# Kernel tuning notes

Hardware: AMD Instinct MI355X
Metric: run time of the kernel (lower is better)

Reference implementation:

```python
import jax, jax.numpy as jnp
import numpy as np

D_MODEL, D_STATE, EXPAND = 1024, 16, 2
D_INNER = EXPAND * D_MODEL
BATCH, SEQ = 4, 4096


def setup_inputs() -> dict:
    key = jax.random.key(0)
    ks = jax.random.split(key, 9)
    s = 0.02
    return {
        "x": jax.random.normal(ks[0], (BATCH, SEQ, D_MODEL), jnp.float32),
        # torch Linear weight [out,in] stored transposed here as [in,out]
        "W_in": jax.random.normal(ks[1], (D_MODEL, 2 * D_INNER), jnp.float32) * s,
        "conv_w": jax.random.normal(ks[2], (D_INNER, 1, 3), jnp.float32) * s,  # depthwise, groups=D_INNER
        "conv_b": jax.random.normal(ks[3], (D_INNER,), jnp.float32) * s,
        "W_B": jax.random.normal(ks[4], (D_INNER, D_STATE), jnp.float32) * s,
        "W_C": jax.random.normal(ks[5], (D_INNER, D_STATE), jnp.float32) * s,
        "A": jax.random.normal(ks[6], (D_STATE,), jnp.float32),
        "D": jnp.ones((D_INNER,), jnp.float32),
        "W_out": jax.random.normal(ks[7], (D_INNER, D_MODEL), jnp.float32) * s,
    }


def reference(x, W_in, conv_w, conv_b, W_B, W_C, A, D, W_out):
    d_inner = conv_w.shape[0]
    # input projection and split into main / residual gate paths
    xr = jnp.einsum("bld,de->ble", x, W_in)  # [B, L, 2*d_inner]
    x_main, res = xr[..., :d_inner], xr[..., d_inner:]
    # depthwise conv1d along seq (kernel 3, pad 1)
    xc = jax.lax.conv_general_dilated(
        x_main.transpose(0, 2, 1), conv_w, (1,), [(1, 1)],
        dimension_numbers=("NCH", "OIH", "NCH"), feature_group_count=d_inner)
    xc = (xc + conv_b[None, :, None]).transpose(0, 2, 1)  # [B, L, d_inner]
    xc = jax.nn.silu(xc)
    # selective-scan inputs
    Bt = jnp.einsum("bli,is->bls", xc, W_B)  # [B, L, d_state]
    Ct = jnp.einsum("bli,is->bls", xc, W_C)
    decay = jnp.exp(-jax.nn.softplus(A))  # exp(A_diag), [d_state]

    def step(state, bc):
        b_t, c_t = bc
        state = state * decay + b_t  # i=0: zeros*decay + B[0] == B[0]
        return state, jnp.sum(state * c_t, axis=-1)  # scalar per batch

    _, ys = jax.lax.scan(step, jnp.zeros_like(Bt[:, 0]),
                         (Bt.transpose(1, 0, 2), Ct.transpose(1, 0, 2)))
    ys = ys.T  # [B, L]
    y = ys[..., None] + xc * D  # broadcast scan output across d_inner
    y = y * jax.nn.silu(res)
    return jnp.einsum("bli,id->bld", y, W_out)
```

## Files before the change

### kernel.cpp

```cpp
#include <hip/hip_runtime.h>


typedef _Float16 half8 __attribute__((ext_vector_type(8)));
typedef float floatx4 __attribute__((ext_vector_type(4)));

#define D_MODEL 1024
#define D_INNER 2048
#define SEQ     4096
#define NBATCH  4
#define NROWS   (NBATCH * SEQ)
#define CHUNK   16
#define NCHUNK  (SEQ / CHUNK)
#define NTASK   (NBATCH * NCHUNK)

__device__ __forceinline__ void async16(_Float16* lds, const _Float16* g) {
    __builtin_amdgcn_global_load_lds((const __attribute__((address_space(1))) void*)g,
                                     (__attribute__((address_space(3))) void*)lds, 16, 0, 0);
}

__device__ __forceinline__ float siluf(float x) {
    return x / (1.f + __expf(-x));
}

__device__ __forceinline__ float decay_of(const float* A, int s) {
    return __expf(-log1pf(__expf(A[s])));
}


__global__ __launch_bounds__(256) void convert_f32_f16(const float* __restrict__ src,
                                                       _Float16* __restrict__ dst) {
    size_t idx = ((size_t)blockIdx.x * 256 + threadIdx.x) * 8;
    float4 a = *(const float4*)(src + idx);
    float4 b = *(const float4*)(src + idx + 4);
    half8 o = {(_Float16)a.x, (_Float16)a.y, (_Float16)a.z, (_Float16)a.w,
               (_Float16)b.x, (_Float16)b.y, (_Float16)b.z, (_Float16)b.w};
    *(half8*)(dst + idx) = o;
}

__global__ __launch_bounds__(256) void transpose_to_f16(const float* __restrict__ src,
                                                        _Float16* __restrict__ dst,
                                                        int K, int N) {
    __shared__ float tile[32][33];
    int n0 = blockIdx.x * 32, k0 = blockIdx.y * 32;
    int x = threadIdx.x, y = threadIdx.y;
#pragma unroll
    for (int r = 0; r < 32; r += 8)
        tile[y + r][x] = src[(size_t)(k0 + y + r) * N + (n0 + x)];
    __syncthreads();
#pragma unroll
    for (int r = 0; r < 32; r += 8)
        dst[(size_t)(n0 + y + r) * K + (k0 + x)] = (_Float16)tile[x][y + r];
}

__global__ __launch_bounds__(256) void convert_wbct(const float* __restrict__ WB,
                                                    const float* __restrict__ WC,
                                                    _Float16* __restrict__ WBCT) {
    int idx = blockIdx.x * 256 + threadIdx.x;
    int n = idx >> 11, k = idx & 2047;
    float v = (n < 16) ? WB[k * 16 + n] : WC[k * 16 + (n - 16)];
    WBCT[idx] = (_Float16)v;
}


__device__ __forceinline__ void stage_half(const _Float16* __restrict__ src, int K,
                                           int rowBase, int k0, _Float16* ldsHalf) {
    const int tid = threadIdx.x;
    const int sr = tid >> 3, wid = tid >> 6;
    const int lc = ((tid & 7) ^ (sr & 7)) << 3;
#pragma unroll
    for (int r = 0; r < 2; r++) {
        const _Float16* g = src + (size_t)(rowBase + r * 64 + sr) * K + (k0 + lc);
        async16(ldsHalf + r * 4096 + wid * 512, g);
    }
}

__device__ __forceinline__ void loadA8(half8 af[4][2], const _Float16* p,
                                       int sw0, int sw1) {
#pragma unroll
    for (int m = 0; m < 4; m++) {
        af[m][0] = *(const half8*)(p + m * 1024 + sw0);
        af[m][1] = *(const half8*)(p + m * 1024 + sw1);
    }
}

__device__ __forceinline__ void loadB4(half8 bf[2][2], const _Float16* p,
                                       int sw0, int sw1) {
#pragma unroll
    for (int n = 0; n < 2; n++) {
        bf[n][0] = *(const half8*)(p + n * 1024 + sw0);
        bf[n][1] = *(const half8*)(p + n * 1024 + sw1);
    }
}

#define GP_MMA(CB, BF)                                                                  \
    __builtin_amdgcn_s_barrier();                                                       \
    __builtin_amdgcn_s_setprio(1);                                                      \
    _Pragma("unroll") for (int s = 0; s < 2; s++)                                       \
        _Pragma("unroll") for (int m = 0; m < 4; m++)                                   \
            _Pragma("unroll") for (int n = 0; n < 2; n++)                               \
                acc[m][(CB) * 2 + n] = __builtin_amdgcn_mfma_f32_16x16x32_f16(          \
                    af[m][s], (BF)[n][s], acc[m][(CB) * 2 + n], 0, 0, 0);               \
    __builtin_amdgcn_s_setprio(0);                                                      \
    __builtin_amdgcn_s_barrier();

template <typename OutT, int NC, int RT>
__global__ __launch_bounds__(512, 2) void gemm256(const _Float16* __restrict__ A,
                                                  const _Float16* __restrict__ BT,
                                                  OutT* __restrict__ C,
                                                  int M, int N, int K) {
    __shared__ __align__(16) _Float16 smem[4 * 16384];
    _Float16* const AsBase = smem;
    _Float16* const BsBase = smem + 32768;

    const int tid = threadIdx.x;
    const int wid = tid >> 6, lane = tid & 63;
    const int wm = wid >> 1, wn = wid & 1;
    const int fr = lane & 15, q = lane >> 4, frq = fr & 7;
    const int sw0 = (q ^ frq) << 3;
    const int sw1 = ((4 + q) ^ frq) << 3;
    const int aB0 = (wm * 64 + fr) * 64;
    const int bB0 = (wn * 128 + fr) * 64;

    const int b = blockIdx.x;
    const int col0 = (b % NC) * 256;
    const int rowBase = (b / NC) * (RT * 256);
    const int NT = K >> 6;

    half8 af[4][2], bfA[2][2], bfB[2][2];

    stage_half(A,  K, rowBase,       0, AsBase);
    stage_half(A,  K, rowBase + 128, 0, AsBase + 8192);
    stage_half(BT, K, col0,          0, BsBase);
    stage_half(BT, K, col0 + 128,    0, BsBase + 8192);
    stage_half(A,  K, rowBase,      64, AsBase + 16384);
    asm volatile("s_waitcnt vmcnt(2)" ::: "memory");
    __builtin_amdgcn_s_barrier();
    asm volatile("" ::: "memory");
    loadB4(bfA, BsBase + bB0, sw0, sw1);
    loadA8(af, AsBase + aB0, sw0, sw1);

    for (int rt = 0; rt < RT; ++rt) {
        const int row0 = rowBase + rt * 256;
        floatx4 acc[4][8] = {};

        for (int t = 0; t < NT; ++t) {
            _Float16* Ab  = AsBase + ((t & 1) << 14);
            _Float16* Bb  = BsBase + ((t & 1) << 14);
            _Float16* Abn = AsBase + (((t + 1) & 1) << 14);
            _Float16* Bbn = BsBase + (((t + 1) & 1) << 14);
            const int k1 = (t + 1) << 6, k2 = (t + 2) << 6;
            const bool s1 = (t + 1) < NT, s2 = (t + 2) < NT;

            loadB4(bfB, Bb + bB0 + 2048, sw0, sw1);
            if (s1) {
                stage_half(A,  K, row0 + 128, k1, Abn + 8192);
                stage_half(BT, K, col0,       k1, Bbn);
            }
            GP_MMA(0, bfA);

            loadB4(bfA, Bb + bB0 + 4096, sw0, sw1);
            if (s1) stage_half(BT, K, col0 + 128, k1, Bbn + 8192);
            GP_MMA(1, bfB);

            loadB4(bfB, Bb + bB0 + 6144, sw0, sw1);
            if (s2) stage_half(A, K, row0, k2, Ab);
            GP_MMA(2, bfA);

            if (s2) {
                asm volatile("s_waitcnt vmcnt(2)" ::: "memory");
            } else if (s1) {
                asm volatile("s_waitcnt vmcnt(0)" ::: "memory");
            }
            __builtin_amdgcn_s_barrier();
            asm volatile("" ::: "memory");
            if (s1) loadB4(bfA, Bbn + bB0, sw0, sw1);
            __builtin_amdgcn_s_setprio(1);
#pragma unroll
            for (int s = 0; s < 2; s++)
#pragma unroll
                for (int m = 0; m < 4; m++)
#pragma unroll
                    for (int n = 0; n < 2; n++)
                        acc[m][6 + n] = __builtin_amdgcn_mfma_f32_16x16x32_f16(
                            af[m][s], bfB[n][s], acc[m][6 + n], 0, 0, 0);
            __builtin_amdgcn_s_setprio(0);
            if (s1) loadA8(af, Abn + aB0, sw0, sw1);
            __builtin_amdgcn_s_barrier();
        }

        if (rt + 1 < RT) {
            const int row0n = row0 + 256;
            stage_half(A,  K, row0n,       0, AsBase);
            stage_half(A,  K, row0n + 128, 0, AsBase + 8192);
            stage_half(BT, K, col0,        0, BsBase);
            stage_half(BT, K, col0 + 128,  0, BsBase + 8192);
            stage_half(A,  K, row0n,      64, AsBase + 16384);
            asm volatile("s_waitcnt vmcnt(2)" ::: "memory");
            __builtin_amdgcn_s_barrier();
            asm volatile("" ::: "memory");
            loadB4(bfA, BsBase + bB0, sw0, sw1);
            loadA8(af, AsBase + aB0, sw0, sw1);
        }

        const int er = (lane >> 4) * 4, ec = lane & 15;
#pragma unroll
        for (int mi = 0; mi < 4; mi++)
#pragma unroll
            for (int cj = 0; cj < 8; cj++)
#pragma unroll
                for (int r = 0; r < 4; r++) {
                    int row = row0 + wm * 64 + mi * 16 + er + r;
                    int col = col0 + wn * 128 + cj * 16 + ec;
                    C[(size_t)row * N + col] = (OutT)acc[mi][cj][r];
                }
    }
}

__global__ __launch_bounds__(256) void conv_bc_fin(const _Float16* __restrict__ xr,
                                                   const float* __restrict__ cw,
                                                   const float* __restrict__ cb,
                                                   const _Float16* __restrict__ WBCT,
                                                   const float* __restrict__ A,
                                                   _Float16* __restrict__ xc,
                                                   float* __restrict__ BtCt,
                                                   float* __restrict__ fin) {
    __shared__ __align__(16) _Float16 As[4 * 32 * 128];
    const int tid = threadIdx.x, wid = tid >> 6, lane = tid & 63;
    const int row0 = blockIdx.x * 32;
    const int l0 = row0 & (SEQ - 1);
    const int cg = lane & 15;
    const int rg = lane >> 4;
    const int fr = lane & 15, q = lane >> 4;
    _Float16* As_w = As + wid * 4096;
    const int r0 = rg * 8;

    floatx4 acc[2][2] = {};

    for (int t = 0; t < 4; t++) {
        const int kbase = wid * 512 + t * 128;
        const int gcol = kbase + cg * 8;
        float w0[8], w1[8], w2[8], bb[8];
#pragma unroll
        for (int j = 0; j < 8; j++) {
            w0[j] = cw[(gcol + j) * 3];
            w1[j] = cw[(gcol + j) * 3 + 1];
            w2[j] = cw[(gcol + j) * 3 + 2];
            bb[j] = cb[gcol + j];
        }
        half8 prev = {}, cur, nxt;
        if (!(l0 == 0 && rg == 0))
            prev = *(const half8*)(xr + (size_t)(row0 + r0 - 1) * 4096 + gcol);
        cur = *(const half8*)(xr + (size_t)(row0 + r0) * 4096 + gcol);
#pragma unroll
        for (int r = 0; r < 8; r++) {
            if (r == 7 && rg == 3 && l0 + 32 == SEQ) {
                half8 z = {};
                nxt = z;
            } else {
                nxt = *(const half8*)(xr + (size_t)(row0 + r0 + r + 1) * 4096 + gcol);
            }
            half8 o;
#pragma unroll
            for (int j = 0; j < 8; j++) {
                float a = (float)prev[j] * w0[j] + (float)cur[j] * w1[j] +
                          (float)nxt[j] * w2[j] + bb[j];
                o[j] = (_Float16)siluf(a);
            }
            const int lrow = r0 + r;
            *(half8*)(xc + (size_t)(row0 + lrow) * D_INNER + gcol) = o;
            *(half8*)(As_w + lrow * 128 + ((cg ^ (lrow & 7)) * 8)) = o;
            prev = cur;
            cur = nxt;
        }
#pragma unroll
        for (int ks = 0; ks < 4; ks++) {
            half8 af[2], bf[2];
#pragma unroll
            for (int rt = 0; rt < 2; rt++)
                af[rt] = *(const half8*)(As_w + (rt * 16 + fr) * 128 +
                                         (((ks * 4 + q) ^ (fr & 7)) * 8));
#pragma unroll
            for (int ot = 0; ot < 2; ot++)
                bf[ot] = *(const half8*)(WBCT + (size_t)(ot * 16 + fr) * D_INNER +
                                         kbase + ks * 32 + q * 8);
#pragma unroll
            for (int rt = 0; rt < 2; rt++)
#pragma unroll
                for (int ot = 0; ot < 2; ot++)
                    acc[rt][ot] = __builtin_amdgcn_mfma_f32_16x16x32_f16(af[rt], bf[ot], acc[rt][ot], 0, 0, 0);
        }
    }

    __syncthreads();
    float* red = (float*)As;
    float* btl = (float*)As + 4096;
    const int er = (lane >> 4) * 4, ec = lane & 15;
#pragma unroll
    for (int rt = 0; rt < 2; rt++)
#pragma unroll
        for (int ot = 0; ot < 2; ot++)
#pragma unroll
            for (int rr = 0; rr < 4; rr++)
                red[wid * 1024 + (rt * 16 + er + rr) * 32 + ot * 16 + ec] = acc[rt][ot][rr];
    __syncthreads();
#pragma unroll
    for (int i = 0; i < 4; i++) {
        int idx = i * 256 + tid;
        float v = red[idx] + red[1024 + idx] + red[2048 + idx] + red[3072 + idx];
        btl[idx] = v;
        BtCt[(size_t)row0 * 32 + idx] = v;
    }
    __syncthreads();
    if (tid < 32) {
        const int ch = tid >> 4, s = tid & 15;
        const float decay = decay_of(A, s);
        float st = 0.f;
#pragma unroll
        for (int r = 0; r < CHUNK; r++)
            st = st * decay + btl[(ch * 16 + r) * 32 + s];
        fin[((row0 >> 4) + ch) * 16 + s] = st;
    }
}

__global__ __launch_bounds__(64) void scan_p2(const float* __restrict__ fin,
                                              const float* __restrict__ A,
                                              float* __restrict__ carry) {
    int t = threadIdx.x;
    int b = t >> 4, s = t & 15;
    float decay = decay_of(A, s);
    float d16 = decay;
#pragma unroll
    for (int k = 0; k < 4; k++) d16 *= d16;
    float cy = 0.f;
#pragma unroll 8
    for (int c = 0; c < NCHUNK; c++) {
        int idx = ((b * NCHUNK) + c) * 16 + s;
        carry[idx] = cy;
        cy = cy * d16 + fin[idx];
    }
}

__global__ __launch_bounds__(256) void scan_p3_fuse(const float* __restrict__ BtCt,
                                                    const float* __restrict__ A,
                                                    const float* __restrict__ carry,
                                                    const float* __restrict__ D,
                                                    const _Float16* __restrict__ xr,
                                                    _Float16* __restrict__ xc) {
    __shared__ float ysl[CHUNK];
    const int task = blockIdx.x;
    const int b = task >> 8, c = task & (NCHUNK - 1);
    const int row0 = b * SEQ + c * CHUNK;
    const int tid = threadIdx.x;

    if (tid < 16) {
        const int s = tid;
        const float decay = decay_of(A, s);
        size_t r = (size_t)row0 * 32;
        float bt[CHUNK], ct[CHUNK];
#pragma unroll
        for (int j = 0; j < CHUNK; j++) {
            bt[j] = BtCt[r + (size_t)j * 32 + s];
            ct[j] = BtCt[r + (size_t)j * 32 + 16 + s];
        }
        float st = carry[task * 16 + s];
        float yv[CHUNK];
#pragma unroll
        for (int j = 0; j < CHUNK; j++) {
            st = st * decay + bt[j];
            yv[j] = st * ct[j];
        }
#pragma unroll
        for (int j = 0; j < CHUNK; j++) {
            float y = yv[j];
            y += __shfl_xor(y, 1, 16);
            y += __shfl_xor(y, 2, 16);
            y += __shfl_xor(y, 4, 16);
            y += __shfl_xor(y, 8, 16);
            if (s == 0) ysl[j] = y;
        }
    }
    __syncthreads();

#pragma unroll
    for (int it = 0; it < 16; it++) {
        int chunk = it * 256 + tid;
        int rl = chunk >> 8;
        int colb = (chunk & 255) * 8;
        size_t row = (size_t)(row0 + rl);
        float yv = ysl[rl];
        half8 x8 = *(const half8*)(xc + row * D_INNER + colb);
        half8 r8 = *(const half8*)(xr + row * 4096 + 2048 + colb);
        float4 d0 = *(const float4*)(D + colb);
        float4 d1 = *(const float4*)(D + colb + 4);
        half8 o;
        float dd[8] = {d0.x, d0.y, d0.z, d0.w, d1.x, d1.y, d1.z, d1.w};
#pragma unroll
        for (int j = 0; j < 8; j++) {
            float y = yv + (float)x8[j] * dd[j];
            o[j] = (_Float16)(y * siluf((float)r8[j]));
        }
        *(half8*)(xc + row * D_INNER + colb) = o;
    }
}

extern "C" void kernel_launch(void* const* d_in, const int* in_sizes, int n_in,
                              void* d_out, int out_size, void* d_ws, size_t ws_size,
                              hipStream_t stream) {
    const float* x      = (const float*)d_in[0];
    const float* W_in   = (const float*)d_in[1];
    const float* conv_w = (const float*)d_in[2];
    const float* conv_b = (const float*)d_in[3];
    const float* W_B    = (const float*)d_in[4];
    const float* W_C    = (const float*)d_in[5];
    const float* A      = (const float*)d_in[6];
    const float* D      = (const float*)d_in[7];
    const float* W_out  = (const float*)d_in[8];
    float* out = (float*)d_out;

    char* ws = (char*)d_ws;
    size_t off = 0;
    auto alloc = [&](size_t bytes) { size_t o = off; off += (bytes + 255) & ~(size_t)255; return o; };
    _Float16* xh    = (_Float16*)(ws + alloc((size_t)NROWS * D_MODEL * 2));
    _Float16* WinT  = (_Float16*)(ws + alloc((size_t)4096 * 1024 * 2));
    _Float16* WoutT = (_Float16*)(ws + alloc((size_t)1024 * 2048 * 2));
    _Float16* WBCT  = (_Float16*)(ws + alloc((size_t)32 * 2048 * 2));
    _Float16* xr    = (_Float16*)(ws + alloc((size_t)NROWS * 4096 * 2));
    _Float16* xc    = (_Float16*)(ws + alloc((size_t)NROWS * D_INNER * 2));
    float*    BtCt  = (float*)(ws + alloc((size_t)NROWS * 32 * 4));
    float*    fin   = (float*)(ws + alloc((size_t)NTASK * 16 * 4));
    float*    carry = (float*)(ws + alloc((size_t)NTASK * 16 * 4));

    convert_f32_f16<<<(NROWS * D_MODEL) / (256 * 8), 256, 0, stream>>>(x, xh);
    transpose_to_f16<<<dim3(4096 / 32, 1024 / 32), dim3(32, 8), 0, stream>>>(W_in, WinT, 1024, 4096);
    transpose_to_f16<<<dim3(1024 / 32, 2048 / 32), dim3(32, 8), 0, stream>>>(W_out, WoutT, 2048, 1024);
    convert_wbct<<<(32 * 2048) / 256, 256, 0, stream>>>(W_B, W_C, WBCT);
    gemm256<_Float16, 16, 4><<<256, 512, 0, stream>>>(xh, WinT, xr, NROWS, 4096, 1024);
    conv_bc_fin<<<NROWS / 32, 256, 0, stream>>>(xr, conv_w, conv_b, WBCT, A, xc, BtCt, fin);
    scan_p2<<<1, 64, 0, stream>>>(fin, A, carry);
    scan_p3_fuse<<<NTASK, 256, 0, stream>>>(BtCt, A, carry, D, xr, xc);
    gemm256<float, 4, 1><<<256, 512, 0, stream>>>(xc, WoutT, out, NROWS, 1024, 2048);
}
```

Measured before the change: 428.1 us.

## Restructure GEMM main loop into two half-tile MMA phases with unified fragments

The GEMM inner loop moves from four MMA phases with ping-pong B fragment registers and cross-iteration prefetch of A/B fragments to two phases. Each phase loads a 4-wide B fragment set, and A fragments are loaded at the start of each k-tile instead of prefetched from the previous one. Barriers become inline-asm s_barrier, and the epilogue store now runs before restaging for the next row tile. This lowers register pressure and barrier count, but LDS fragment loads are no longer overlapped with the prior tile's MFMAs.

```diff
diff --git a/kernel.cpp b/kernel.cpp
--- a/kernel.cpp
+++ b/kernel.cpp
@@ -26,6 +26,8 @@
     return __expf(-log1pf(__expf(A[s])));
 }
 
+#define BAR() asm volatile("s_barrier" ::: "memory")
+
 
 __global__ __launch_bounds__(256) void convert_f32_f16(const float* __restrict__ src,
                                                        _Float16* __restrict__ dst) {
@@ -83,25 +85,25 @@
     }
 }
 
-__device__ __forceinline__ void loadB4(half8 bf[2][2], const _Float16* p,
+__device__ __forceinline__ void loadB8(half8 bf[4][2], const _Float16* p,
                                        int sw0, int sw1) {
 #pragma unroll
-    for (int n = 0; n < 2; n++) {
+    for (int n = 0; n < 4; n++) {
         bf[n][0] = *(const half8*)(p + n * 1024 + sw0);
         bf[n][1] = *(const half8*)(p + n * 1024 + sw1);
     }
 }
 
-#define GP_MMA(CB, BF)                                                                  \
-    __builtin_amdgcn_s_barrier();                                                       \
+#define GP_MMA2(CBP)                                                                    \
+    BAR();                                                                              \
     __builtin_amdgcn_s_setprio(1);                                                      \
     _Pragma("unroll") for (int s = 0; s < 2; s++)                                       \
         _Pragma("unroll") for (int m = 0; m < 4; m++)                                   \
-            _Pragma("unroll") for (int n = 0; n < 2; n++)                               \
-                acc[m][(CB) * 2 + n] = __builtin_amdgcn_mfma_f32_16x16x32_f16(          \
-                    af[m][s], (BF)[n][s], acc[m][(CB) * 2 + n], 0, 0, 0);               \
+            _Pragma("unroll") for (int n = 0; n < 4; n++)                               \
+                acc[m][(CBP) * 4 + n] = __builtin_amdgcn_mfma_f32_16x16x32_f16(         \
+                    af[m][s], bf[n][s], acc[m][(CBP) * 4 + n], 0, 0, 0);                \
     __builtin_amdgcn_s_setprio(0);                                                      \
-    __builtin_amdgcn_s_barrier();
+    BAR();
 
 template <typename OutT, int NC, int RT>
 __global__ __launch_bounds__(512, 2) void gemm256(const _Float16* __restrict__ A,
@@ -126,7 +128,7 @@
     const int rowBase = (b / NC) * (RT * 256);
     const int NT = K >> 6;
 
-    half8 af[4][2], bfA[2][2], bfB[2][2];
+    half8 af[4][2], bf[4][2];
 
     stage_half(A,  K, rowBase,       0, AsBase);
     stage_half(A,  K, rowBase + 128, 0, AsBase + 8192);
@@ -134,10 +136,7 @@
     stage_half(BT, K, col0 + 128,    0, BsBase + 8192);
     stage_half(A,  K, rowBase,      64, AsBase + 16384);
     asm volatile("s_waitcnt vmcnt(2)" ::: "memory");
-    __builtin_amdgcn_s_barrier();
-    asm volatile("" ::: "memory");
-    loadB4(bfA, BsBase + bB0, sw0, sw1);
-    loadA8(af, AsBase + aB0, sw0, sw1);
+    BAR();
 
     for (int rt = 0; rt < RT; ++rt) {
         const int row0 = rowBase + rt * 256;
@@ -151,42 +150,36 @@
             const int k1 = (t + 1) << 6, k2 = (t + 2) << 6;
             const bool s1 = (t + 1) < NT, s2 = (t + 2) < NT;
 
-            loadB4(bfB, Bb + bB0 + 2048, sw0, sw1);
+            loadA8(af, Ab + aB0, sw0, sw1);
+            loadB8(bf, Bb + bB0, sw0, sw1);
             if (s1) {
                 stage_half(A,  K, row0 + 128, k1, Abn + 8192);
                 stage_half(BT, K, col0,       k1, Bbn);
             }
-            GP_MMA(0, bfA);
-
-            loadB4(bfA, Bb + bB0 + 4096, sw0, sw1);
+            GP_MMA2(0);
+
+            loadB8(bf, Bb + bB0 + 4096, sw0, sw1);
             if (s1) stage_half(BT, K, col0 + 128, k1, Bbn + 8192);
-            GP_MMA(1, bfB);
-
-            loadB4(bfB, Bb + bB0 + 6144, sw0, sw1);
             if (s2) stage_half(A, K, row0, k2, Ab);
-            GP_MMA(2, bfA);
-
             if (s2) {
                 asm volatile("s_waitcnt vmcnt(2)" ::: "memory");
             } else if (s1) {
                 asm volatile("s_waitcnt vmcnt(0)" ::: "memory");
             }
-            __builtin_amdgcn_s_barrier();
-            asm volatile("" ::: "memory");
-            if (s1) loadB4(bfA, Bbn + bB0, sw0, sw1);
-            __builtin_amdgcn_s_setprio(1);
-#pragma unroll
-            for (int s = 0; s < 2; s++)
-#pragma unroll
-                for (int m = 0; m < 4; m++)
-#pragma unroll
-                    for (int n = 0; n < 2; n++)
-                        acc[m][6 + n] = __builtin_amdgcn_mfma_f32_16x16x32_f16(
-                            af[m][s], bfB[n][s], acc[m][6 + n], 0, 0, 0);
-            __builtin_amdgcn_s_setprio(0);
-            if (s1) loadA8(af, Abn + aB0, sw0, sw1);
-            __builtin_amdgcn_s_barrier();
-        }
+            GP_MMA2(1);
+        }
+
+        const int er = (lane >> 4) * 4, ec = lane & 15;
+#pragma unroll
+        for (int mi = 0; mi < 4; mi++)
+#pragma unroll
+            for (int cj = 0; cj < 8; cj++)
+#pragma unroll
+                for (int r = 0; r < 4; r++) {
+                    int row = row0 + wm * 64 + mi * 16 + er + r;
+                    int col = col0 + wn * 128 + cj * 16 + ec;
+                    C[(size_t)row * N + col] = (OutT)acc[mi][cj][r];
+                }
 
         if (rt + 1 < RT) {
             const int row0n = row0 + 256;
@@ -196,23 +189,8 @@
             stage_half(BT, K, col0 + 128,  0, BsBase + 8192);
             stage_half(A,  K, row0n,      64, AsBase + 16384);
             asm volatile("s_waitcnt vmcnt(2)" ::: "memory");
-            __builtin_amdgcn_s_barrier();
-            asm volatile("" ::: "memory");
-            loadB4(bfA, BsBase + bB0, sw0, sw1);
-            loadA8(af, AsBase + aB0, sw0, sw1);
-        }
-
-        const int er = (lane >> 4) * 4, ec = lane & 15;
-#pragma unroll
-        for (int mi = 0; mi < 4; mi++)
-#pragma unroll
-            for (int cj = 0; cj < 8; cj++)
-#pragma unroll
-                for (int r = 0; r < 4; r++) {
-                    int row = row0 + wm * 64 + mi * 16 + er + r;
-                    int col = col0 + wn * 128 + cj * 16 + ec;
-                    C[(size_t)row * N + col] = (OutT)acc[mi][cj][r];
-                }
+            BAR();
+        }
     }
 }
 
```

Result: slower. 450.3 us (+5.2%).
